# Performance work log

Measured on AMD Instinct MI355X. Metric: run time of the kernel, lower is better.

The kernel has to match this reference:

```python
import jax, jax.numpy as jnp
import numpy as np

M, K, N = 8192, 4096, 4096

def setup_inputs() -> dict:
    key = jax.random.key(0)
    k1, k2, k3, k4, k5 = jax.random.split(key, 5)
    # int8-range quantized tensors stored as int32 (int8 values in [-128, 127])
    inp = jax.random.randint(k1, (M, K), -128, 128, dtype=jnp.int32)
    weight = jax.random.randint(k2, (N, K), -128, 128, dtype=jnp.int32)
    bias = jax.random.normal(k3, (N,), dtype=jnp.float32)
    inp_scales = jax.random.uniform(k4, (1,), jnp.float32, 0.01, 0.05)        # per-tensor
    inp_zero_points = jnp.zeros((1,), jnp.int32)                               # symmetric
    weight_scales = jax.random.uniform(k5, (N,), jnp.float32, 0.005, 0.02)     # per-channel
    weight_zero_points = jnp.zeros((N,), jnp.int32)
    return {
        "inp": inp, "weight": weight, "bias": bias,
        "inp_scales": inp_scales, "inp_zero_points": inp_zero_points,
        "weight_scales": weight_scales, "weight_zero_points": weight_zero_points,
    }

def reference(inp, weight, bias, inp_scales, inp_zero_points, weight_scales, weight_zero_points):
    # qdq_linear fallback path: dequantize activation (per-tensor) and weight
    # (per-output-channel), fp32 matmul, add bias. output_dtype=float32,
    # output_scales/zero_points=None => no output requantization.
    x = (inp.astype(jnp.float32) - inp_zero_points.astype(jnp.float32)) * inp_scales  # [M,K]
    w = (weight.astype(jnp.float32) - weight_zero_points[:, None].astype(jnp.float32)) \
        * weight_scales[:, None]                                                      # [N,K]
    return jnp.einsum('mk,nk->mn', x, w) + bias                                       # [M,N]
```

## Files before the change

kernel.cpp:

```cpp
#include <hip/hip_runtime.h>

#define MM 8192
#define NN 4096
#define KK 4096

#define BM 128
#define BN 128
#define BK 64

typedef int int32x4 __attribute__((ext_vector_type(4)));

__device__ __forceinline__ void async_load16(const void* g, void* l) {
  __builtin_amdgcn_global_load_lds(
      (__attribute__((address_space(1))) void*)(void*)g,
      (__attribute__((address_space(3))) void*)l,
      16, 0, 0);
}

__global__ __launch_bounds__(256) void pack_kernel(
    const int* __restrict__ a, const int* __restrict__ w,
    char* __restrict__ a8, char* __restrict__ w8,
    const int* __restrict__ izp, const int* __restrict__ wzp) {
  const long tid = (long)blockIdx.x * 256 + threadIdx.x;
  const long A_VECS = (long)MM * KK / 16;

  const int4* src;
  char* dst;
  int z;
  if (tid < A_VECS) {
    src = (const int4*)a + tid * 4;
    dst = a8 + tid * 16;
    z = izp[0];
  } else {
    long t = tid - A_VECS;
    src = (const int4*)w + t * 4;
    dst = w8 + t * 16;
    z = wzp[t >> 8];
  }

  int4 v0 = src[0], v1 = src[1], v2 = src[2], v3 = src[3];
  union { char c[16]; int4 q; } u;
  u.c[ 0]=(char)(v0.x-z); u.c[ 1]=(char)(v0.y-z); u.c[ 2]=(char)(v0.z-z); u.c[ 3]=(char)(v0.w-z);
  u.c[ 4]=(char)(v1.x-z); u.c[ 5]=(char)(v1.y-z); u.c[ 6]=(char)(v1.z-z); u.c[ 7]=(char)(v1.w-z);
  u.c[ 8]=(char)(v2.x-z); u.c[ 9]=(char)(v2.y-z); u.c[10]=(char)(v2.z-z); u.c[11]=(char)(v2.w-z);
  u.c[12]=(char)(v3.x-z); u.c[13]=(char)(v3.y-z); u.c[14]=(char)(v3.z-z); u.c[15]=(char)(v3.w-z);
  *(int4*)dst = u.q;
}

__global__ __launch_bounds__(256, 2) void qgemm_kernel(
    const char* __restrict__ A8, const char* __restrict__ W8,
    float* __restrict__ out,
    const float* __restrict__ bias,
    const float* __restrict__ is_ptr,
    const float* __restrict__ wscale) {
  __shared__ __attribute__((aligned(16))) char As[BM * BK];
  __shared__ __attribute__((aligned(16))) char Bs[BN * BK];

  int pid = blockIdx.x;
  pid = (pid & 7) * 256 + (pid >> 3);
  const int group  = pid >> 8;
  const int within = pid & 255;
  const int bm = group * 8 + (within & 7);
  const int bn = within >> 3;

  const int tid  = threadIdx.x;
  const int wave = tid >> 6;
  const int lane = tid & 63;
  const int wm = (wave >> 1) * 64;
  const int wn = (wave & 1) * 64;

  const int row_q = lane & 15;
  const int quad  = lane >> 4;
  const int swz   = quad ^ (row_q >> 2);

  const int s_row = lane >> 2;
  const int s_sub = (lane & 3) ^ ((lane >> 4) & 3);
  const long a_row0 = (long)(bm * BM + wave * 16 + s_row);
  const long a_row1 = (long)(bm * BM + (wave + 4) * 16 + s_row);
  const long b_row0 = (long)(bn * BN + wave * 16 + s_row);
  const long b_row1 = (long)(bn * BN + (wave + 4) * 16 + s_row);
  const char* a_src0 = A8 + a_row0 * KK + s_sub * 16;
  const char* a_src1 = A8 + a_row1 * KK + s_sub * 16;
  const char* b_src0 = W8 + b_row0 * KK + s_sub * 16;
  const char* b_src1 = W8 + b_row1 * KK + s_sub * 16;
  char* a_dst0 = As + wave * 1024;
  char* a_dst1 = As + (wave + 4) * 1024;
  char* b_dst0 = Bs + wave * 1024;
  char* b_dst1 = Bs + (wave + 4) * 1024;

  const char* a_rd = As + (wm + row_q) * BK + swz * 16;
  const char* b_rd = Bs + (wn + row_q) * BK + swz * 16;

  int32x4 acc[4][4];
#pragma unroll
  for (int mi = 0; mi < 4; ++mi)
#pragma unroll
    for (int ni = 0; ni < 4; ++ni) acc[mi][ni] = (int32x4)0;

  for (int kk = 0; kk < KK; kk += BK) {
    async_load16(a_src0 + kk, a_dst0);
    async_load16(a_src1 + kk, a_dst1);
    async_load16(b_src0 + kk, b_dst0);
    async_load16(b_src1 + kk, b_dst1);
    __syncthreads();

    int32x4 afrag[4], bfrag[4];
#pragma unroll
    for (int mi = 0; mi < 4; ++mi)
      afrag[mi] = *(const int32x4*)(a_rd + mi * 16 * BK);
#pragma unroll
    for (int ni = 0; ni < 4; ++ni)
      bfrag[ni] = *(const int32x4*)(b_rd + ni * 16 * BK);

#pragma unroll
    for (int mi = 0; mi < 4; ++mi)
#pragma unroll
      for (int ni = 0; ni < 4; ++ni)
        acc[mi][ni] = __builtin_amdgcn_mfma_i32_16x16x64_i8(
            afrag[mi], bfrag[ni], acc[mi][ni], 0, 0, 0);

    __syncthreads();
  }

  const float is0 = is_ptr[0];
  const int row_base = bm * BM + wm + quad * 4;
  const int col_base = bn * BN + wn + row_q;
#pragma unroll
  for (int ni = 0; ni < 4; ++ni) {
    const int col = col_base + ni * 16;
    const float s = is0 * wscale[col];
    const float b = bias[col];
#pragma unroll
    for (int mi = 0; mi < 4; ++mi) {
      const int row = row_base + mi * 16;
#pragma unroll
      for (int r = 0; r < 4; ++r) {
        out[(long)(row + r) * NN + col] = (float)acc[mi][ni][r] * s + b;
      }
    }
  }
}

extern "C" void kernel_launch(void* const* d_in, const int* in_sizes, int n_in,
                              void* d_out, int out_size, void* d_ws, size_t ws_size,
                              hipStream_t stream) {
  const int*   inp    = (const int*)d_in[0];
  const int*   weight = (const int*)d_in[1];
  const float* bias   = (const float*)d_in[2];
  const float* iscale = (const float*)d_in[3];
  const int*   izp    = (const int*)d_in[4];
  const float* wscale = (const float*)d_in[5];
  const int*   wzp    = (const int*)d_in[6];
  float* out = (float*)d_out;

  char* a8 = (char*)d_ws;
  char* w8 = a8 + (size_t)MM * KK;

  pack_kernel<<<12288, 256, 0, stream>>>(inp, weight, a8, w8, izp, wzp);

  qgemm_kernel<<<2048, 256, 0, stream>>>(a8, w8, out, bias, iscale, wscale);
}
```

Measured before the change: 426.8 us.

## Double K-tile depth to 128 and pack one int4 per thread

The GEMM's K tile grows from 64 to 128, so each iteration loads twice the data into LDS and runs two MFMA half-steps. This halves the number of barrier pairs per output tile, using a new 8-row swizzle for the 128-byte rows. The pack kernel now has each thread convert one int4 into 4 bytes instead of four int4s into 16, with four times as many blocks. LDS use doubles, which could affect occupancy at two blocks per CU, and there is still no double buffering.

```diff
diff --git a/kernel.cpp b/kernel.cpp
--- a/kernel.cpp
+++ b/kernel.cpp
@@ -6,7 +6,7 @@
 
 #define BM 128
 #define BN 128
-#define BK 64
+#define BK 128
 
 typedef int int32x4 __attribute__((ext_vector_type(4)));
 
@@ -22,29 +22,29 @@
     char* __restrict__ a8, char* __restrict__ w8,
     const int* __restrict__ izp, const int* __restrict__ wzp) {
   const long tid = (long)blockIdx.x * 256 + threadIdx.x;
-  const long A_VECS = (long)MM * KK / 16;
+  const long A_T = (long)MM * KK / 4;
 
   const int4* src;
-  char* dst;
+  int* dst;
   int z;
-  if (tid < A_VECS) {
-    src = (const int4*)a + tid * 4;
-    dst = a8 + tid * 16;
+  if (tid < A_T) {
+    src = (const int4*)a + tid;
+    dst = (int*)a8 + tid;
     z = izp[0];
   } else {
-    long t = tid - A_VECS;
-    src = (const int4*)w + t * 4;
-    dst = w8 + t * 16;
-    z = wzp[t >> 8];
+    long t = tid - A_T;
+    src = (const int4*)w + t;
+    dst = (int*)w8 + t;
+    z = wzp[t >> 10];
   }
 
-  int4 v0 = src[0], v1 = src[1], v2 = src[2], v3 = src[3];
-  union { char c[16]; int4 q; } u;
-  u.c[ 0]=(char)(v0.x-z); u.c[ 1]=(char)(v0.y-z); u.c[ 2]=(char)(v0.z-z); u.c[ 3]=(char)(v0.w-z);
-  u.c[ 4]=(char)(v1.x-z); u.c[ 5]=(char)(v1.y-z); u.c[ 6]=(char)(v1.z-z); u.c[ 7]=(char)(v1.w-z);
-  u.c[ 8]=(char)(v2.x-z); u.c[ 9]=(char)(v2.y-z); u.c[10]=(char)(v2.z-z); u.c[11]=(char)(v2.w-z);
-  u.c[12]=(char)(v3.x-z); u.c[13]=(char)(v3.y-z); u.c[14]=(char)(v3.z-z); u.c[15]=(char)(v3.w-z);
-  *(int4*)dst = u.q;
+  int4 v = *src;
+  union { char c[4]; int q; } u;
+  u.c[0] = (char)(v.x - z);
+  u.c[1] = (char)(v.y - z);
+  u.c[2] = (char)(v.z - z);
+  u.c[3] = (char)(v.w - z);
+  *dst = u.q;
 }
 
 __global__ __launch_bounds__(256, 2) void qgemm_kernel(
@@ -69,27 +69,27 @@
   const int wm = (wave >> 1) * 64;
   const int wn = (wave & 1) * 64;
 
+  const int srow = lane >> 3;
+  const int ssub = (lane & 7) ^ srow;
+  const char* a_src[4];
+  const char* b_src[4];
+  char* a_dst[4];
+  char* b_dst[4];
+#pragma unroll
+  for (int j = 0; j < 4; ++j) {
+    const int c = wave + j * 4;
+    a_src[j] = A8 + (long)(bm * BM + c * 8 + srow) * KK + ssub * 16;
+    b_src[j] = W8 + (long)(bn * BN + c * 8 + srow) * KK + ssub * 16;
+    a_dst[j] = As + c * 1024;
+    b_dst[j] = Bs + c * 1024;
+  }
+
   const int row_q = lane & 15;
   const int quad  = lane >> 4;
-  const int swz   = quad ^ (row_q >> 2);
-
-  const int s_row = lane >> 2;
-  const int s_sub = (lane & 3) ^ ((lane >> 4) & 3);
-  const long a_row0 = (long)(bm * BM + wave * 16 + s_row);
-  const long a_row1 = (long)(bm * BM + (wave + 4) * 16 + s_row);
-  const long b_row0 = (long)(bn * BN + wave * 16 + s_row);
-  const long b_row1 = (long)(bn * BN + (wave + 4) * 16 + s_row);
-  const char* a_src0 = A8 + a_row0 * KK + s_sub * 16;
-  const char* a_src1 = A8 + a_row1 * KK + s_sub * 16;
-  const char* b_src0 = W8 + b_row0 * KK + s_sub * 16;
-  const char* b_src1 = W8 + b_row1 * KK + s_sub * 16;
-  char* a_dst0 = As + wave * 1024;
-  char* a_dst1 = As + (wave + 4) * 1024;
-  char* b_dst0 = Bs + wave * 1024;
-  char* b_dst1 = Bs + (wave + 4) * 1024;
-
-  const char* a_rd = As + (wm + row_q) * BK + swz * 16;
-  const char* b_rd = Bs + (wn + row_q) * BK + swz * 16;
+  const int psub0 = quad ^ (row_q & 7);
+  const int psub1 = psub0 ^ 4;
+  const char* a_rd = As + (wm + row_q) * BK;
+  const char* b_rd = Bs + (wn + row_q) * BK;
 
   int32x4 acc[4][4];
 #pragma unroll
@@ -98,26 +98,31 @@
     for (int ni = 0; ni < 4; ++ni) acc[mi][ni] = (int32x4)0;
 
   for (int kk = 0; kk < KK; kk += BK) {
-    async_load16(a_src0 + kk, a_dst0);
-    async_load16(a_src1 + kk, a_dst1);
-    async_load16(b_src0 + kk, b_dst0);
-    async_load16(b_src1 + kk, b_dst1);
+#pragma unroll
+    for (int j = 0; j < 4; ++j) {
+      async_load16(a_src[j] + kk, a_dst[j]);
+      async_load16(b_src[j] + kk, b_dst[j]);
+    }
     __syncthreads();
 
-    int32x4 afrag[4], bfrag[4];
 #pragma unroll
-    for (int mi = 0; mi < 4; ++mi)
-      afrag[mi] = *(const int32x4*)(a_rd + mi * 16 * BK);
+    for (int h = 0; h < 2; ++h) {
+      const int ps = (h == 0) ? psub0 : psub1;
+      int32x4 afrag[4], bfrag[4];
 #pragma unroll
-    for (int ni = 0; ni < 4; ++ni)
-      bfrag[ni] = *(const int32x4*)(b_rd + ni * 16 * BK);
+      for (int mi = 0; mi < 4; ++mi)
+        afrag[mi] = *(const int32x4*)(a_rd + mi * 16 * BK + ps * 16);
+#pragma unroll
+      for (int ni = 0; ni < 4; ++ni)
+        bfrag[ni] = *(const int32x4*)(b_rd + ni * 16 * BK + ps * 16);
 
 #pragma unroll
-    for (int mi = 0; mi < 4; ++mi)
+      for (int mi = 0; mi < 4; ++mi)
 #pragma unroll
-      for (int ni = 0; ni < 4; ++ni)
-        acc[mi][ni] = __builtin_amdgcn_mfma_i32_16x16x64_i8(
-            afrag[mi], bfrag[ni], acc[mi][ni], 0, 0, 0);
+        for (int ni = 0; ni < 4; ++ni)
+          acc[mi][ni] = __builtin_amdgcn_mfma_i32_16x16x64_i8(
+              afrag[mi], bfrag[ni], acc[mi][ni], 0, 0, 0);
+    }
 
     __syncthreads();
   }
@@ -156,7 +161,7 @@
   char* a8 = (char*)d_ws;
   char* w8 = a8 + (size_t)MM * KK;
 
-  pack_kernel<<<12288, 256, 0, stream>>>(inp, weight, a8, w8, izp, wzp);
+  pack_kernel<<<49152, 256, 0, stream>>>(inp, weight, a8, w8, izp, wzp);
 
   qgemm_kernel<<<2048, 256, 0, stream>>>(a8, w8, out, bias, iscale, wscale);
 }
```

Measured after the change: 403.8 us. -5.4%, faster.
